# Kernel optimization log

Measured on AMD Instinct MI355X. Metric: run time of the kernel, lower is better.

The kernel has to match this reference:

```python
import jax, jax.numpy as jnp
import numpy as np

N = 50000      # total nodes
E = 800000     # total edges
IN = 8         # in_channels
H = 16         # hidden_dim
OUT = 16       # out_channels
B = 64         # number of graphs in batch


def _glorot(k, shape):
    fan_out, fan_in = shape[0], shape[1]
    lim = float(np.sqrt(6.0 / (fan_in + fan_out)))
    return jax.random.uniform(k, shape, jnp.float32, -lim, lim)


def setup_inputs() -> dict:
    key = jax.random.key(0)
    ks = jax.random.split(key, 12)
    return {
        "x": jax.random.normal(ks[0], (N, IN), jnp.float32),
        "edge_attr": jax.random.uniform(ks[1], (E, 1), jnp.float32),
        # edge MLP 1: Linear(1, H) -> ReLU -> Linear(H, IN*H)
        "W_e1a": _glorot(ks[2], (H, 1)), "b_e1a": jnp.zeros((H,), jnp.float32),
        "W_e1b": _glorot(ks[3], (IN * H, H)), "b_e1b": jnp.zeros((IN * H,), jnp.float32),
        "root1": _glorot(ks[4], (IN, H)), "bias1": jnp.zeros((H,), jnp.float32),
        # edge MLP 2: Linear(1, H) -> ReLU -> Linear(H, H*OUT)
        "W_e2a": _glorot(ks[5], (H, 1)), "b_e2a": jnp.zeros((H,), jnp.float32),
        "W_e2b": _glorot(ks[6], (H * OUT, H)), "b_e2b": jnp.zeros((H * OUT,), jnp.float32),
        "root2": _glorot(ks[7], (H, OUT)), "bias2": jnp.zeros((OUT,), jnp.float32),
        "edge_index": jax.random.randint(ks[8], (2, E), 0, N, jnp.int32),
        "batch": jnp.sort(jax.random.randint(ks[9], (N,), 0, B, jnp.int32)),
    }


def _segment_mean(vals, idx, num_segments):
    s = jax.ops.segment_sum(vals, idx, num_segments=num_segments)
    cnt = jax.ops.segment_sum(jnp.ones((vals.shape[0],), vals.dtype), idx,
                              num_segments=num_segments)
    return s / jnp.maximum(cnt, 1.0)[:, None]


def _nnconv(x, src, dst, edge_attr, Wa, ba, Wb, bb, root, bias, din, dout):
    # edge MLP -> per-edge weight matrix [E, din, dout]
    he = jax.nn.relu(edge_attr @ Wa.T + ba)
    We = (he @ Wb.T + bb).reshape(-1, din, dout)
    # per-edge matmul on gathered source features, scatter-mean to dst
    msg = jnp.einsum('ei,eio->eo', x[src], We)
    agg = _segment_mean(msg, dst, x.shape[0])
    return agg + x @ root + bias


def reference(x, edge_attr, W_e1a, b_e1a, W_e1b, b_e1b, root1, bias1,
              W_e2a, b_e2a, W_e2b, b_e2b, root2, bias2, edge_index, batch):
    src, dst = edge_index[0], edge_index[1]
    h = jax.nn.relu(_nnconv(x, src, dst, edge_attr,
                            W_e1a, b_e1a, W_e1b, b_e1b, root1, bias1, IN, H))
    h = jax.nn.relu(_nnconv(h, src, dst, edge_attr,
                            W_e2a, b_e2a, W_e2b, b_e2b, root2, bias2, H, OUT))
    g = _segment_mean(h, batch, B)  # global mean pool per graph
    return (h, g, batch)
```

## Files before the change

kernel.cpp:

```cpp
#include <hip/hip_runtime.h>
#include <hip/hip_bf16.h>

typedef __bf16 bf16;
typedef __bf16 bf16x8 __attribute__((ext_vector_type(8)));
typedef float  f32x4  __attribute__((ext_vector_type(4)));


__global__ void node_pre1(const float* __restrict__ x,
                          const float* __restrict__ root1,
                          const float* __restrict__ bias1,
                          float* __restrict__ r1, int N)
{
    int t = blockIdx.x * blockDim.x + threadIdx.x;
    int v = t >> 4, o = t & 15;
    if (v >= N) return;
    float racc = 0.f;
#pragma unroll
    for (int i = 0; i < 8; ++i)
        racc += x[v * 8 + i] * root1[i * 16 + o];
    r1[v * 16 + o] = racc + bias1[o];
}

__global__ void __launch_bounds__(256, 8)
edge_l1(const float* __restrict__ x,
        const float* __restrict__ ea,
        const int*   __restrict__ eidx,
        const float* __restrict__ W_e1a, const float* __restrict__ b_e1a,
        const float* __restrict__ W_e1b, const float* __restrict__ b_e1b,
        float* __restrict__ agg, int* __restrict__ cnt,
        int E, int ntiles)
{
    const int lane = threadIdx.x & 63;
    const int m = lane & 15;
    const int q = lane >> 4;
    const int wave   = blockIdx.x * (blockDim.x >> 6) + (threadIdx.x >> 6);
    const int nwaves = gridDim.x * (blockDim.x >> 6);

    bf16x8 bfrag[4];
#pragma unroll
    for (int c = 0; c < 4; ++c)
#pragma unroll
        for (int t = 0; t < 8; ++t)
            bfrag[c][t] = (bf16)W_e1b[(t * 16 + m) * 16 + (c * 4 + q)];
    bf16x8 bfrag5 = {};
    if (q == 0)
#pragma unroll
        for (int t = 0; t < 8; ++t)
            bfrag5[t] = (bf16)b_e1b[t * 16 + m];

    for (int tile = wave; tile < ntiles; tile += nwaves) {
        int e = tile * 16 + m;
        int s = eidx[e];
        int d = eidx[E + e];
        float t_ea = ea[e];

        float he[4];
#pragma unroll
        for (int c = 0; c < 4; ++c) {
            int j = c * 4 + q;
            float h = W_e1a[j] * t_ea + b_e1a[j];
            he[c] = h > 0.f ? h : 0.f;
        }

        const float4* xp = (const float4*)(x + (size_t)s * 8);
        float4 x0 = xp[0], x1 = xp[1];
        float xv[8] = {x0.x, x0.y, x0.z, x0.w, x1.x, x1.y, x1.z, x1.w};

        f32x4 acc = {0.f, 0.f, 0.f, 0.f};
#pragma unroll
        for (int c = 0; c < 4; ++c) {
            bf16x8 afrag;
#pragma unroll
            for (int t = 0; t < 8; ++t) afrag[t] = (bf16)(he[c] * xv[t]);
            acc = __builtin_amdgcn_mfma_f32_16x16x32_bf16(afrag, bfrag[c], acc, 0, 0, 0);
        }
        {
            bf16x8 a5 = {};
            if (q == 0)
#pragma unroll
                for (int t = 0; t < 8; ++t) a5[t] = (bf16)xv[t];
            acc = __builtin_amdgcn_mfma_f32_16x16x32_bf16(a5, bfrag5, acc, 0, 0, 0);
        }

        if (q == 0) atomicAdd(&cnt[d], 1);

#pragma unroll
        for (int reg = 0; reg < 4; ++reg) {
            int d_r = __shfl(d, q * 4 + reg, 64);
            atomicAdd(&agg[d_r * 16 + m], acc[reg]);
        }
    }
}

__global__ void node_fin1(const float* __restrict__ agg, const int* __restrict__ cnt,
                          const float* __restrict__ r1,
                          const float* __restrict__ root2,
                          const float* __restrict__ bias2,
                          float* __restrict__ h1, float* __restrict__ r2, int N)
{
    int t = blockIdx.x * blockDim.x + threadIdx.x;
    int v = t >> 4, o = t & 15;
    if (v >= N) return;
    float c = (float)cnt[v]; c = c > 1.f ? c : 1.f;
    float h = agg[v * 16 + o] / c + r1[v * 16 + o];
    h = h > 0.f ? h : 0.f;
    h1[v * 16 + o] = h;
    float racc = 0.f;
#pragma unroll
    for (int i = 0; i < 16; ++i)
        racc += __shfl(h, i, 16) * root2[i * 16 + o];
    r2[v * 16 + o] = racc + bias2[o];
}

__global__ void __launch_bounds__(256, 8)
edge_l2(const float* __restrict__ h1g,
        const float* __restrict__ ea,
        const int*   __restrict__ eidx,
        const float* __restrict__ W_e2a, const float* __restrict__ b_e2a,
        const float* __restrict__ W_e2b, const float* __restrict__ b_e2b,
        float* __restrict__ agg, int E, int ntiles)
{
    const int lane = threadIdx.x & 63;
    const int m = lane & 15;
    const int q = lane >> 4;
    const int qh = q >> 1;
    const int ql = q & 1;
    const int wave   = blockIdx.x * (blockDim.x >> 6) + (threadIdx.x >> 6);
    const int nwaves = gridDim.x * (blockDim.x >> 6);

    bf16x8 bfrag[8];
#pragma unroll
    for (int c = 0; c < 8; ++c) {
        int j = c * 2 + qh;
#pragma unroll
        for (int t = 0; t < 8; ++t)
            bfrag[c][t] = (bf16)W_e2b[((ql * 8 + t) * 16 + m) * 16 + j];
    }
    bf16x8 bfrag5 = {};
    if (q < 2)
#pragma unroll
        for (int t = 0; t < 8; ++t)
            bfrag5[t] = (bf16)b_e2b[(q * 8 + t) * 16 + m];

    for (int tile = wave; tile < ntiles; tile += nwaves) {
        int e = tile * 16 + m;
        int s = eidx[e];
        int d = eidx[E + e];
        float t_ea = ea[e];

        float he[8];
#pragma unroll
        for (int c = 0; c < 8; ++c) {
            int j = c * 2 + qh;
            float h = W_e2a[j] * t_ea + b_e2a[j];
            he[c] = h > 0.f ? h : 0.f;
        }

        const float4* hp = (const float4*)(h1g + (size_t)s * 16 + ql * 8);
        float4 h0 = hp[0], h1v = hp[1];
        float hv[8] = {h0.x, h0.y, h0.z, h0.w, h1v.x, h1v.y, h1v.z, h1v.w};

        f32x4 acc = {0.f, 0.f, 0.f, 0.f};
#pragma unroll
        for (int c = 0; c < 8; ++c) {
            bf16x8 afrag;
#pragma unroll
            for (int t = 0; t < 8; ++t) afrag[t] = (bf16)(he[c] * hv[t]);
            acc = __builtin_amdgcn_mfma_f32_16x16x32_bf16(afrag, bfrag[c], acc, 0, 0, 0);
        }
        {
            bf16x8 a5 = {};
            if (q < 2)
#pragma unroll
                for (int t = 0; t < 8; ++t) a5[t] = (bf16)hv[t];
            acc = __builtin_amdgcn_mfma_f32_16x16x32_bf16(a5, bfrag5, acc, 0, 0, 0);
        }

#pragma unroll
        for (int reg = 0; reg < 4; ++reg) {
            int d_r = __shfl(d, q * 4 + reg, 64);
            atomicAdd(&agg[d_r * 16 + m], acc[reg]);
        }
    }
}

__global__ void node_fin2(const float* __restrict__ agg, const int* __restrict__ cnt,
                          const float* __restrict__ r2, const int* __restrict__ batch,
                          float* __restrict__ out_h, float* __restrict__ out_b, int N)
{
    int t = blockIdx.x * blockDim.x + threadIdx.x;
    int v = t >> 4, o = t & 15;
    if (v >= N) return;
    float c = (float)cnt[v]; c = c > 1.f ? c : 1.f;
    float h = agg[v * 16 + o] / c + r2[v * 16 + o];
    h = h > 0.f ? h : 0.f;
    out_h[v * 16 + o] = h;
    if (o == 0) out_b[v] = (float)batch[v];
}

__global__ void pool_seg(const float* __restrict__ h, const int* __restrict__ batch,
                         float* __restrict__ out_g, int N)
{
    const int b = blockIdx.x;
    int lo = 0, hi = N;
    while (lo < hi) { int mid = (lo + hi) >> 1; if (batch[mid] < b) lo = mid + 1; else hi = mid; }
    const int start = lo;
    hi = N;
    while (lo < hi) { int mid = (lo + hi) >> 1; if (batch[mid] < b + 1) lo = mid + 1; else hi = mid; }
    const int end = lo;

    const int ch = threadIdx.x & 15, grp = threadIdx.x >> 4;
    float acc = 0.f;
    for (int v = start + grp; v < end; v += 16)
        acc += h[(size_t)v * 16 + ch];

    __shared__ float red[256];
    red[threadIdx.x] = acc;
    __syncthreads();
#pragma unroll
    for (int s = 128; s >= 16; s >>= 1) {
        if (threadIdx.x < s) red[threadIdx.x] += red[threadIdx.x + s];
        __syncthreads();
    }
    if (threadIdx.x < 16) {
        float c = (float)(end - start); c = c > 1.f ? c : 1.f;
        out_g[b * 16 + threadIdx.x] = red[threadIdx.x] / c;
    }
}

extern "C" void kernel_launch(void* const* d_in, const int* in_sizes, int n_in,
                              void* d_out, int out_size, void* d_ws, size_t ws_size,
                              hipStream_t stream)
{
    const float* x     = (const float*)d_in[0];
    const float* ea    = (const float*)d_in[1];
    const float* W_e1a = (const float*)d_in[2];
    const float* b_e1a = (const float*)d_in[3];
    const float* W_e1b = (const float*)d_in[4];
    const float* b_e1b = (const float*)d_in[5];
    const float* root1 = (const float*)d_in[6];
    const float* bias1 = (const float*)d_in[7];
    const float* W_e2a = (const float*)d_in[8];
    const float* b_e2a = (const float*)d_in[9];
    const float* W_e2b = (const float*)d_in[10];
    const float* b_e2b = (const float*)d_in[11];
    const float* root2 = (const float*)d_in[12];
    const float* bias2 = (const float*)d_in[13];
    const int*   eidx  = (const int*)d_in[14];
    const int*   batch = (const int*)d_in[15];

    const int E  = in_sizes[1];
    const int N  = in_sizes[15];
    const int Bg = (out_size - N * 16 - N) / 16;

    char* ws = (char*)d_ws;
    size_t off = 0;
    int*   cnt  = (int*)(ws + off);   off += (size_t)N * 4;
    float* agg1 = (float*)(ws + off); off += (size_t)N * 16 * 4;
    float* agg2 = (float*)(ws + off); off += (size_t)N * 16 * 4;
    size_t zero_bytes = off;
    float* h1 = (float*)(ws + off); off += (size_t)N * 16 * 4;
    float* r1 = (float*)(ws + off); off += (size_t)N * 16 * 4;
    float* r2 = (float*)(ws + off); off += (size_t)N * 16 * 4;

    hipMemsetAsync(d_ws, 0, zero_bytes, stream);

    int nodeBlocks = (N * 16 + 255) / 256;
    int ntiles = E / 16;

    node_pre1<<<nodeBlocks, 256, 0, stream>>>(x, root1, bias1, r1, N);
    edge_l1<<<2048, 256, 0, stream>>>(x, ea, eidx, W_e1a, b_e1a, W_e1b, b_e1b,
                                      agg1, cnt, E, ntiles);
    node_fin1<<<nodeBlocks, 256, 0, stream>>>(agg1, cnt, r1, root2, bias2,
                                              h1, r2, N);
    edge_l2<<<2048, 256, 0, stream>>>(h1, ea, eidx, W_e2a, b_e2a, W_e2b, b_e2b,
                                      agg2, E, ntiles);

    float* out_h = (float*)d_out;
    float* out_g = out_h + (size_t)N * 16;
    float* out_b = out_g + (size_t)Bg * 16;
    node_fin2<<<nodeBlocks, 256, 0, stream>>>(agg2, cnt, r2, batch, out_h,
                                              out_b, N);
    pool_seg<<<Bg, 256, 0, stream>>>(out_h, batch, out_g, N);
}
```

Before: 328.8 us.

## Counting-sort edges by destination and run-length merge scatter atomics

Adds a per-call counting sort of edges by destination node: a degree histogram, a single-block prefix scan, and an atomic-cursor scatter into sorted src/dst/edge_attr arrays. Both edge kernels then read the sorted arrays. Within each 16-edge tile they walk the rows with shuffles and sum consecutive rows that share a destination, issuing one atomic per run instead of one per edge per channel. The degree histogram also replaces the in-kernel count atomics. The aim is far fewer global float atomics, at the cost of three extra preprocessing kernels (one of them single-block and serial), a serial 16-step shuffle loop, and a smaller edge-kernel grid without launch bounds.

```diff
diff --git a/kernel.cpp b/kernel.cpp
--- a/kernel.cpp
+++ b/kernel.cpp
@@ -5,6 +5,52 @@
 typedef __bf16 bf16x8 __attribute__((ext_vector_type(8)));
 typedef float  f32x4  __attribute__((ext_vector_type(4)));
 
+
+__global__ void hist_deg(const int* __restrict__ eidx, int* __restrict__ deg, int E)
+{
+    int e = blockIdx.x * blockDim.x + threadIdx.x;
+    if (e < E) atomicAdd(&deg[eidx[E + e]], 1);
+}
+
+__global__ void scan_deg(const int* __restrict__ deg, int* __restrict__ cursor, int N)
+{
+    __shared__ int part[1024];
+    const int t = threadIdx.x;
+    const int CH = (N + 1023) >> 10;
+    const int base = t * CH;
+    int sum = 0;
+    for (int k = 0; k < CH; ++k) {
+        int i = base + k;
+        if (i < N) sum += deg[i];
+    }
+    part[t] = sum;
+    __syncthreads();
+    for (int off = 1; off < 1024; off <<= 1) {
+        int add = (t >= off) ? part[t - off] : 0;
+        __syncthreads();
+        part[t] += add;
+        __syncthreads();
+    }
+    int run = part[t] - sum;
+    for (int k = 0; k < CH; ++k) {
+        int i = base + k;
+        if (i < N) { cursor[i] = run; run += deg[i]; }
+    }
+}
+
+__global__ void scatter_edges(const int* __restrict__ eidx, const float* __restrict__ ea,
+                              int* __restrict__ cursor,
+                              int* __restrict__ src_s, int* __restrict__ dst_s,
+                              float* __restrict__ ea_s, int E)
+{
+    int e = blockIdx.x * blockDim.x + threadIdx.x;
+    if (e >= E) return;
+    int d = eidx[E + e];
+    int p = atomicAdd(&cursor[d], 1);
+    src_s[p] = eidx[e];
+    dst_s[p] = d;
+    ea_s[p]  = ea[e];
+}
 
 __global__ void node_pre1(const float* __restrict__ x,
                           const float* __restrict__ root1,
@@ -21,14 +67,12 @@
     r1[v * 16 + o] = racc + bias1[o];
 }
 
-__global__ void __launch_bounds__(256, 8)
-edge_l1(const float* __restrict__ x,
-        const float* __restrict__ ea,
-        const int*   __restrict__ eidx,
-        const float* __restrict__ W_e1a, const float* __restrict__ b_e1a,
-        const float* __restrict__ W_e1b, const float* __restrict__ b_e1b,
-        float* __restrict__ agg, int* __restrict__ cnt,
-        int E, int ntiles)
+__global__ void edge_l1(const float* __restrict__ x,
+                        const float* __restrict__ ea_s,
+                        const int*   __restrict__ src_s, const int* __restrict__ dst_s,
+                        const float* __restrict__ W_e1a, const float* __restrict__ b_e1a,
+                        const float* __restrict__ W_e1b, const float* __restrict__ b_e1b,
+                        float* __restrict__ agg, int ntiles)
 {
     const int lane = threadIdx.x & 63;
     const int m = lane & 15;
@@ -50,9 +94,9 @@
 
     for (int tile = wave; tile < ntiles; tile += nwaves) {
         int e = tile * 16 + m;
-        int s = eidx[e];
-        int d = eidx[E + e];
-        float t_ea = ea[e];
+        int s = src_s[e];
+        int d = dst_s[e];
+        float t_ea = ea_s[e];
 
         float he[4];
 #pragma unroll
@@ -82,17 +126,23 @@
             acc = __builtin_amdgcn_mfma_f32_16x16x32_bf16(a5, bfrag5, acc, 0, 0, 0);
         }
 
-        if (q == 0) atomicAdd(&cnt[d], 1);
-
-#pragma unroll
-        for (int reg = 0; reg < 4; ++reg) {
-            int d_r = __shfl(d, q * 4 + reg, 64);
-            atomicAdd(&agg[d_r * 16 + m], acc[reg]);
-        }
-    }
-}
-
-__global__ void node_fin1(const float* __restrict__ agg, const int* __restrict__ cnt,
+        int   run_d   = __shfl(d, 0, 64);
+        float run_sum = 0.f;
+#pragma unroll
+        for (int r = 0; r < 16; ++r) {
+            int   dr = __shfl(d, r, 64);
+            float vr = __shfl(acc[r & 3], ((r >> 2) << 4) + m, 64);
+            if (dr != run_d) {
+                if (q == 0) atomicAdd(&agg[(size_t)run_d * 16 + m], run_sum);
+                run_sum = 0.f; run_d = dr;
+            }
+            run_sum += vr;
+        }
+        if (q == 0) atomicAdd(&agg[(size_t)run_d * 16 + m], run_sum);
+    }
+}
+
+__global__ void node_fin1(const float* __restrict__ agg, const int* __restrict__ deg,
                           const float* __restrict__ r1,
                           const float* __restrict__ root2,
                           const float* __restrict__ bias2,
@@ -101,7 +151,7 @@
     int t = blockIdx.x * blockDim.x + threadIdx.x;
     int v = t >> 4, o = t & 15;
     if (v >= N) return;
-    float c = (float)cnt[v]; c = c > 1.f ? c : 1.f;
+    float c = (float)deg[v]; c = c > 1.f ? c : 1.f;
     float h = agg[v * 16 + o] / c + r1[v * 16 + o];
     h = h > 0.f ? h : 0.f;
     h1[v * 16 + o] = h;
@@ -112,13 +162,12 @@
     r2[v * 16 + o] = racc + bias2[o];
 }
 
-__global__ void __launch_bounds__(256, 8)
-edge_l2(const float* __restrict__ h1g,
-        const float* __restrict__ ea,
-        const int*   __restrict__ eidx,
-        const float* __restrict__ W_e2a, const float* __restrict__ b_e2a,
-        const float* __restrict__ W_e2b, const float* __restrict__ b_e2b,
-        float* __restrict__ agg, int E, int ntiles)
+__global__ void edge_l2(const float* __restrict__ h1g,
+                        const float* __restrict__ ea_s,
+                        const int*   __restrict__ src_s, const int* __restrict__ dst_s,
+                        const float* __restrict__ W_e2a, const float* __restrict__ b_e2a,
+                        const float* __restrict__ W_e2b, const float* __restrict__ b_e2b,
+                        float* __restrict__ agg, int ntiles)
 {
     const int lane = threadIdx.x & 63;
     const int m = lane & 15;
@@ -144,9 +193,9 @@
 
     for (int tile = wave; tile < ntiles; tile += nwaves) {
         int e = tile * 16 + m;
-        int s = eidx[e];
-        int d = eidx[E + e];
-        float t_ea = ea[e];
+        int s = src_s[e];
+        int d = dst_s[e];
+        float t_ea = ea_s[e];
 
         float he[8];
 #pragma unroll
@@ -176,22 +225,30 @@
             acc = __builtin_amdgcn_mfma_f32_16x16x32_bf16(a5, bfrag5, acc, 0, 0, 0);
         }
 
-#pragma unroll
-        for (int reg = 0; reg < 4; ++reg) {
-            int d_r = __shfl(d, q * 4 + reg, 64);
-            atomicAdd(&agg[d_r * 16 + m], acc[reg]);
-        }
-    }
-}
-
-__global__ void node_fin2(const float* __restrict__ agg, const int* __restrict__ cnt,
+        int   run_d   = __shfl(d, 0, 64);
+        float run_sum = 0.f;
+#pragma unroll
+        for (int r = 0; r < 16; ++r) {
+            int   dr = __shfl(d, r, 64);
+            float vr = __shfl(acc[r & 3], ((r >> 2) << 4) + m, 64);
+            if (dr != run_d) {
+                if (q == 0) atomicAdd(&agg[(size_t)run_d * 16 + m], run_sum);
+                run_sum = 0.f; run_d = dr;
+            }
+            run_sum += vr;
+        }
+        if (q == 0) atomicAdd(&agg[(size_t)run_d * 16 + m], run_sum);
+    }
+}
+
+__global__ void node_fin2(const float* __restrict__ agg, const int* __restrict__ deg,
                           const float* __restrict__ r2, const int* __restrict__ batch,
                           float* __restrict__ out_h, float* __restrict__ out_b, int N)
 {
     int t = blockIdx.x * blockDim.x + threadIdx.x;
     int v = t >> 4, o = t & 15;
     if (v >= N) return;
-    float c = (float)cnt[v]; c = c > 1.f ? c : 1.f;
+    float c = (float)deg[v]; c = c > 1.f ? c : 1.f;
     float h = agg[v * 16 + o] / c + r2[v * 16 + o];
     h = h > 0.f ? h : 0.f;
     out_h[v * 16 + o] = h;
@@ -255,10 +312,14 @@
 
     char* ws = (char*)d_ws;
     size_t off = 0;
-    int*   cnt  = (int*)(ws + off);   off += (size_t)N * 4;
+    int*   deg  = (int*)(ws + off);   off += (size_t)N * 4;
     float* agg1 = (float*)(ws + off); off += (size_t)N * 16 * 4;
     float* agg2 = (float*)(ws + off); off += (size_t)N * 16 * 4;
     size_t zero_bytes = off;
+    int*   cursor = (int*)(ws + off); off += (size_t)N * 4;
+    int*   src_s  = (int*)(ws + off); off += (size_t)E * 4;
+    int*   dst_s  = (int*)(ws + off); off += (size_t)E * 4;
+    float* ea_s   = (float*)(ws + off); off += (size_t)E * 4;
     float* h1 = (float*)(ws + off); off += (size_t)N * 16 * 4;
     float* r1 = (float*)(ws + off); off += (size_t)N * 16 * 4;
     float* r2 = (float*)(ws + off); off += (size_t)N * 16 * 4;
@@ -266,20 +327,26 @@
     hipMemsetAsync(d_ws, 0, zero_bytes, stream);
 
     int nodeBlocks = (N * 16 + 255) / 256;
+    int edgeBlocks = (E + 255) / 256;
     int ntiles = E / 16;
 
+    hist_deg<<<edgeBlocks, 256, 0, stream>>>(eidx, deg, E);
+    scan_deg<<<1, 1024, 0, stream>>>(deg, cursor, N);
+    scatter_edges<<<edgeBlocks, 256, 0, stream>>>(eidx, ea, cursor,
+                                                  src_s, dst_s, ea_s, E);
+
     node_pre1<<<nodeBlocks, 256, 0, stream>>>(x, root1, bias1, r1, N);
-    edge_l1<<<2048, 256, 0, stream>>>(x, ea, eidx, W_e1a, b_e1a, W_e1b, b_e1b,
-                                      agg1, cnt, E, ntiles);
-    node_fin1<<<nodeBlocks, 256, 0, stream>>>(agg1, cnt, r1, root2, bias2,
+    edge_l1<<<1024, 256, 0, stream>>>(x, ea_s, src_s, dst_s,
+                                      W_e1a, b_e1a, W_e1b, b_e1b, agg1, ntiles);
+    node_fin1<<<nodeBlocks, 256, 0, stream>>>(agg1, deg, r1, root2, bias2,
                                               h1, r2, N);
-    edge_l2<<<2048, 256, 0, stream>>>(h1, ea, eidx, W_e2a, b_e2a, W_e2b, b_e2b,
-                                      agg2, E, ntiles);
+    edge_l2<<<1024, 256, 0, stream>>>(h1, ea_s, src_s, dst_s,
+                                      W_e2a, b_e2a, W_e2b, b_e2b, agg2, ntiles);
 
     float* out_h = (float*)d_out;
     float* out_g = out_h + (size_t)N * 16;
     float* out_b = out_g + (size_t)Bg * 16;
-    node_fin2<<<nodeBlocks, 256, 0, stream>>>(agg2, cnt, r2, batch, out_h,
+    node_fin2<<<nodeBlocks, 256, 0, stream>>>(agg2, deg, r2, batch, out_h,
                                               out_b, N);
     pool_seg<<<Bg, 256, 0, stream>>>(out_h, batch, out_g, N);
 }
```

New measurement: 399.3 us. 1.21x slower.
